# Optimization experiments

Measured on AMD Instinct MI355X. Metric: run time of the kernel, lower is better.

Reference implementation:

```python
import jax, jax.numpy as jnp
import numpy as np

B, S, E, H = 2, 2048, 1024, 16
HD = E // H


def setup_inputs() -> dict:
    key = jax.random.key(0)
    ks = jax.random.split(key, 9)
    s = 1.0 / np.sqrt(E)
    return {
        "x": jax.random.normal(ks[0], (B, S, E), dtype=jnp.float32),
        "wq": jax.random.uniform(ks[1], (E, E), jnp.float32, -s, s),
        "bq": jax.random.uniform(ks[2], (E,), jnp.float32, -s, s),
        "wk": jax.random.uniform(ks[3], (E, E), jnp.float32, -s, s),
        "bk": jax.random.uniform(ks[4], (E,), jnp.float32, -s, s),
        "wv": jax.random.uniform(ks[5], (E, E), jnp.float32, -s, s),
        "bv": jax.random.uniform(ks[6], (E,), jnp.float32, -s, s),
        "wo": jax.random.uniform(ks[7], (E, E), jnp.float32, -s, s),
        "bo": jax.random.uniform(ks[8], (E,), jnp.float32, -s, s),
    }


def reference(x, wq, bq, wk, bk, wv, bv, wo, bo):
    b, s, e = x.shape
    # QKV projections, reshape to [b, h, s, hd]
    def proj(w, bias):
        y = jnp.einsum('bse,ef->bsf', x, w.T) + bias
        return y.reshape(b, s, H, HD).transpose(0, 2, 1, 3)
    q = proj(wq, bq)
    k = proj(wk, bk)
    v = proj(wv, bv)
    score = jnp.einsum('bhqd,bhkd->bhqk', q, k) / jnp.sqrt(jnp.float32(HD))
    # original: exp(x)/sum(exp(x)) + 1e-8  == softmax(x) + 1e-8
    attn = jax.nn.softmax(score, axis=-1) + 1e-8
    out = jnp.einsum('bhqk,bhkd->bhqd', attn, v)
    out = out.transpose(0, 2, 1, 3).reshape(b, s, e)
    return jnp.einsum('bse,ef->bsf', out, wo.T) + bo
```

## Files before the change

### kernel.cpp

```cpp
#include <hip/hip_runtime.h>
#include <hip/hip_bf16.h>
#include <cstdint>

#define SS 2048
#define EE 1024
#define HH 16
#define HDD 64

typedef __attribute__((ext_vector_type(8))) __bf16 bf16x8;
typedef __attribute__((ext_vector_type(4))) float f32x4;

#define MFMA16(a, b, c) __builtin_amdgcn_mfma_f32_16x16x32_bf16((a), (b), (c), 0, 0, 0)

__device__ __forceinline__ unsigned short f2bf(float f) {
    unsigned int u = __builtin_bit_cast(unsigned int, f);
    u += 0x7FFFu + ((u >> 16) & 1u);
    return (unsigned short)(u >> 16);
}

__device__ __forceinline__ void gll16(const unsigned short* g, unsigned short* l) {
    __builtin_amdgcn_global_load_lds(
        (__attribute__((address_space(1))) unsigned int*)g,
        (__attribute__((address_space(3))) unsigned int*)l, 16, 0, 0);
}

__global__ __launch_bounds__(256) void cvt_all(
    const float* __restrict__ x, const float* __restrict__ wq, const float* __restrict__ wk,
    const float* __restrict__ wv, const float* __restrict__ wo,
    unsigned short* __restrict__ xb, unsigned short* __restrict__ wqb, unsigned short* __restrict__ wkb,
    unsigned short* __restrict__ wvb, unsigned short* __restrict__ wob) {
    int idx = blockIdx.x * 256 + threadIdx.x;
    int i4 = idx << 2;
    const float* src;
    unsigned short* dst;
    int off;
    if (i4 < 4194304) { src = x; dst = xb; off = i4; }
    else {
        int w = (i4 - 4194304) >> 20;
        off = (i4 - 4194304) & 1048575;
        if (w == 0) { src = wq; dst = wqb; }
        else if (w == 1) { src = wk; dst = wkb; }
        else if (w == 2) { src = wv; dst = wvb; }
        else { src = wo; dst = wob; }
    }
    float4 v = *(const float4*)&src[off];
    unsigned int p0 = (unsigned int)f2bf(v.x) | ((unsigned int)f2bf(v.y) << 16);
    unsigned int p1 = (unsigned int)f2bf(v.z) | ((unsigned int)f2bf(v.w) << 16);
    uint2 u; u.x = p0; u.y = p1;
    *(uint2*)&dst[off] = u;
}

template <int MODE>
__device__ __forceinline__ void gemm_core(
    const unsigned short* __restrict__ A, const unsigned short* __restrict__ W,
    const float* __restrict__ bias, void* __restrict__ out) {
    __shared__ unsigned short lsA[128 * 32];
    __shared__ unsigned short lsB[128 * 32];
    const int t = threadIdx.x;
    const int lane = t & 63, l15 = lane & 15, quad = lane >> 4;
    const int wave = t >> 6;
    const int wm = (wave >> 1) * 64, wn = (wave & 1) * 64;
    const int bm = blockIdx.y * 128, bn = blockIdx.x * 128;

    const int cg = ((t & 3) ^ ((t >> 3) & 3)) * 8;
    const unsigned short* ga = A + (size_t)(bm + (t >> 2)) * 1024 + cg;
    const unsigned short* gb = W + (size_t)(bn + (t >> 2)) * 1024 + cg;

    f32x4 acc[4][4];
    for (int i = 0; i < 4; i++)
        for (int j = 0; j < 4; j++) acc[i][j] = (f32x4){0.f, 0.f, 0.f, 0.f};

    const int swz = (l15 >> 1) & 3;

    for (int k0 = 0; k0 < 1024; k0 += 32) {
        gll16(ga + k0, &lsA[t * 8]);
        gll16(ga + k0 + 64 * 1024, &lsA[2048 + t * 8]);
        gll16(gb + k0, &lsB[t * 8]);
        gll16(gb + k0 + 64 * 1024, &lsB[2048 + t * 8]);
        __syncthreads();
        bf16x8 af[4], bfr[4];
        for (int i = 0; i < 4; i++)
            af[i] = *(const bf16x8*)&lsA[(wm + i * 16 + l15) * 32 + ((quad ^ swz) * 8)];
        for (int j = 0; j < 4; j++)
            bfr[j] = *(const bf16x8*)&lsB[(wn + j * 16 + l15) * 32 + ((quad ^ swz) * 8)];
        for (int i = 0; i < 4; i++)
            for (int j = 0; j < 4; j++) acc[i][j] = MFMA16(af[i], bfr[j], acc[i][j]);
        __syncthreads();
    }

    for (int j = 0; j < 4; j++) {
        int n = bn + wn + j * 16 + l15;
        float bj = bias[n];
        for (int i = 0; i < 4; i++) {
            int mbase = bm + wm + i * 16 + quad * 4;
            for (int rg = 0; rg < 4; rg++) {
                float val = acc[i][j][rg] + bj;
                int m = mbase + rg;
                if (MODE == 0) {
                    ((unsigned short*)out)[(((size_t)(m >> 11) * HH + (n >> 6)) * SS + (m & 2047)) * HDD + (n & 63)] = f2bf(val);
                } else {
                    ((float*)out)[(size_t)m * 1024 + n] = val;
                }
            }
        }
    }
}

__global__ __launch_bounds__(256) void gemm_qkv(
    const unsigned short* __restrict__ xb,
    const unsigned short* __restrict__ wqb, const unsigned short* __restrict__ wkb,
    const unsigned short* __restrict__ wvb,
    const float* __restrict__ bq, const float* __restrict__ bk, const float* __restrict__ bv,
    unsigned short* qb, unsigned short* kb, unsigned short* vb) {
    const unsigned short* W;
    const float* bias;
    unsigned short* out;
    if (blockIdx.z == 0) { W = wqb; bias = bq; out = qb; }
    else if (blockIdx.z == 1) { W = wkb; bias = bk; out = kb; }
    else { W = wvb; bias = bv; out = vb; }
    gemm_core<0>(xb, W, bias, out);
}

__global__ __launch_bounds__(256) void gemm_out(
    const unsigned short* __restrict__ ob, const unsigned short* __restrict__ wob,
    const float* __restrict__ bo, float* __restrict__ out) {
    gemm_core<1>(ob, wob, bo, out);
}

__global__ __launch_bounds__(256) void transpose_v(
    const unsigned short* __restrict__ vb, unsigned short* __restrict__ vtb) {
    __shared__ unsigned short tile[64 * 66];
    const int t = threadIdx.x;
    const int bh = blockIdx.y, st = blockIdx.x;
    const size_t base = (size_t)bh * (SS * HDD);
    const int c = (t & 7) * 8, r0 = t >> 3;
    for (int it = 0; it < 2; it++) {
        int r = r0 + it * 32;
        uint4 d = *(const uint4*)&vb[base + (size_t)(st * 64 + r) * HDD + c];
        unsigned int* dst = (unsigned int*)&tile[r * 66 + c];
        dst[0] = d.x; dst[1] = d.y; dst[2] = d.z; dst[3] = d.w;
    }
    __syncthreads();
    for (int it = 0; it < 2; it++) {
        int hd = r0 + it * 32;
        unsigned short v0[8];
        for (int k = 0; k < 8; k++) v0[k] = tile[(c + k) * 66 + hd];
        uint4 o;
        o.x = (unsigned int)v0[0] | ((unsigned int)v0[1] << 16);
        o.y = (unsigned int)v0[2] | ((unsigned int)v0[3] << 16);
        o.z = (unsigned int)v0[4] | ((unsigned int)v0[5] << 16);
        o.w = (unsigned int)v0[6] | ((unsigned int)v0[7] << 16);
        *(uint4*)&vtb[base + (size_t)hd * SS + st * 64 + c] = o;
    }
}

#define PSTR 72

__global__ __launch_bounds__(256) void attn_fwd(
    const unsigned short* __restrict__ qb, const unsigned short* __restrict__ kb,
    const unsigned short* __restrict__ vtb, unsigned short* __restrict__ ob) {
    __shared__ unsigned short lsK[64 * 64];
    __shared__ unsigned short lsV[64 * 64];
    __shared__ unsigned short lsP[4 * 32 * PSTR];
    const int t = threadIdx.x, lane = t & 63, l15 = lane & 15, quad = lane >> 4, wave = t >> 6;
    const int bh = blockIdx.y, qt = blockIdx.x;
    const size_t hoff = (size_t)bh * (SS * HDD);
    const float C = 0.125f * 1.44269504088896f;

    bf16x8 qf[2][2];
    const int qrow = qt * 128 + wave * 32;
    for (int i = 0; i < 2; i++)
        for (int ks = 0; ks < 2; ks++) {
            bf16x8 raw = *(const bf16x8*)&qb[hoff + (size_t)(qrow + i * 16 + l15) * HDD + ks * 32 + quad * 8];
            unsigned short tmp[8];
            *(bf16x8*)tmp = raw;
            for (int j = 0; j < 8; j++) {
                float f = __builtin_bit_cast(float, (unsigned int)tmp[j] << 16);
                tmp[j] = f2bf(f * C);
            }
            qf[i][ks] = *(const bf16x8*)tmp;
        }

    unsigned short onesbuf[8];
    for (int j = 0; j < 8; j++) onesbuf[j] = 0x3F80;
    const bf16x8 onesf = *(const bf16x8*)onesbuf;

    f32x4 lacc[2];
    f32x4 o[2][4];
    for (int i = 0; i < 2; i++) {
        lacc[i] = (f32x4){0.f, 0.f, 0.f, 0.f};
        for (int jh = 0; jh < 4; jh++) o[i][jh] = (f32x4){0.f, 0.f, 0.f, 0.f};
    }

    const int cg = (((t & 7) ^ ((t >> 3) & 7))) * 8;
    const unsigned short* gk = kb + hoff + (size_t)(t >> 3) * HDD + cg;
    const unsigned short* gv = vtb + hoff + (size_t)(t >> 3) * SS + cg;
    const int pbase = wave * 32 * PSTR;
    const int sw = l15 & 7;

    for (int kt = 0; kt < 32; kt++) {
        gll16(gk + (size_t)kt * 64 * HDD, &lsK[t * 8]);
        gll16(gk + (size_t)kt * 64 * HDD + 32 * HDD, &lsK[2048 + t * 8]);
        gll16(gv + kt * 64, &lsV[t * 8]);
        gll16(gv + kt * 64 + 32 * SS, &lsV[2048 + t * 8]);
        __syncthreads();

        bf16x8 kfr[4][2];
        for (int j = 0; j < 4; j++)
            for (int ks = 0; ks < 2; ks++)
                kfr[j][ks] = *(const bf16x8*)&lsK[(j * 16 + l15) * 64 + (((ks * 4 + quad) ^ sw) * 8)];

        f32x4 st[4][2];
        for (int j = 0; j < 4; j++)
            for (int i = 0; i < 2; i++) {
                f32x4 z = (f32x4){0.f, 0.f, 0.f, 0.f};
                z = MFMA16(kfr[j][0], qf[i][0], z);
                z = MFMA16(kfr[j][1], qf[i][1], z);
                st[j][i] = z;
            }

        for (int j = 0; j < 4; j++)
            for (int i = 0; i < 2; i++) {
                float e0 = __builtin_amdgcn_exp2f(st[j][i][0]);
                float e1 = __builtin_amdgcn_exp2f(st[j][i][1]);
                float e2 = __builtin_amdgcn_exp2f(st[j][i][2]);
                float e3 = __builtin_amdgcn_exp2f(st[j][i][3]);
                uint2 w;
                w.x = (__builtin_bit_cast(unsigned int, e0) >> 16) |
                      (__builtin_bit_cast(unsigned int, e1) & 0xFFFF0000u);
                w.y = (__builtin_bit_cast(unsigned int, e2) >> 16) |
                      (__builtin_bit_cast(unsigned int, e3) & 0xFFFF0000u);
                *(uint2*)&lsP[pbase + (i * 16 + l15) * PSTR + j * 16 + quad * 4] = w;
            }

        bf16x8 pf[2][2], vf[4][2];
        for (int i = 0; i < 2; i++)
            for (int ks = 0; ks < 2; ks++)
                pf[i][ks] = *(const bf16x8*)&lsP[pbase + (i * 16 + l15) * PSTR + ks * 32 + quad * 8];
        for (int jh = 0; jh < 4; jh++)
            for (int ks = 0; ks < 2; ks++)
                vf[jh][ks] = *(const bf16x8*)&lsV[(jh * 16 + l15) * 64 + (((ks * 4 + quad) ^ sw) * 8)];
        for (int i = 0; i < 2; i++) {
            for (int jh = 0; jh < 4; jh++) {
                o[i][jh] = MFMA16(pf[i][0], vf[jh][0], o[i][jh]);
                o[i][jh] = MFMA16(pf[i][1], vf[jh][1], o[i][jh]);
            }
            lacc[i] = MFMA16(pf[i][0], onesf, lacc[i]);
            lacc[i] = MFMA16(pf[i][1], onesf, lacc[i]);
        }
        __syncthreads();
    }

    const int b = bh >> 4, h = bh & 15;
    for (int i = 0; i < 2; i++)
        for (int rg = 0; rg < 4; rg++) {
            float inv = 1.f / lacc[i][rg];
            int srow = qt * 128 + wave * 32 + i * 16 + quad * 4 + rg;
            size_t rowoff = ((size_t)b * SS + srow) * EE + h * 64;
            for (int jh = 0; jh < 4; jh++)
                ob[rowoff + jh * 16 + l15] = f2bf(o[i][jh][rg] * inv);
        }
}

extern "C" void kernel_launch(void* const* d_in, const int* in_sizes, int n_in,
                              void* d_out, int out_size, void* d_ws, size_t ws_size,
                              hipStream_t stream) {
    const float* x  = (const float*)d_in[0];
    const float* wq = (const float*)d_in[1];
    const float* bq = (const float*)d_in[2];
    const float* wk = (const float*)d_in[3];
    const float* bk = (const float*)d_in[4];
    const float* wv = (const float*)d_in[5];
    const float* bv = (const float*)d_in[6];
    const float* wo = (const float*)d_in[7];
    const float* bo = (const float*)d_in[8];

    char* ws = (char*)d_ws;
    unsigned short* xb  = (unsigned short*)(ws + 0);
    unsigned short* wqb = (unsigned short*)(ws + 8388608);
    unsigned short* wkb = (unsigned short*)(ws + 10485760);
    unsigned short* wvb = (unsigned short*)(ws + 12582912);
    unsigned short* wob = (unsigned short*)(ws + 14680064);
    unsigned short* qb  = (unsigned short*)(ws + 16777216);
    unsigned short* kb  = (unsigned short*)(ws + 25165824);
    unsigned short* vb  = (unsigned short*)(ws + 33554432);
    unsigned short* vtb = (unsigned short*)(ws + 41943040);
    unsigned short* ob  = xb;

    cvt_all<<<8192, 256, 0, stream>>>(x, wq, wk, wv, wo, xb, wqb, wkb, wvb, wob);
    gemm_qkv<<<dim3(8, 32, 3), 256, 0, stream>>>(xb, wqb, wkb, wvb, bq, bk, bv, qb, kb, vb);
    transpose_v<<<dim3(32, 32), 256, 0, stream>>>(vb, vtb);
    attn_fwd<<<dim3(16, 32), 256, 0, stream>>>(qb, kb, vtb, ob);
    gemm_out<<<dim3(8, 32), 256, 0, stream>>>(ob, wob, bo, (float*)d_out);
}
```

Before: 222.8 us.

## Fuse V transpose into QKV GEMM epilogue, remap blocks, narrow output GEMM tiles

The QKV GEMM now writes V directly in transposed [b,h,hd,s] layout using packed 4-element stores, which removes the separate transpose_v kernel and its round trip through global memory. All three main kernels switch to 1D grids with a block-index remapping that spreads consecutive blocks across 8 groups, likely to balance work across XCDs and L2 caches. The output GEMM uses 128x64 tiles, giving 512 blocks instead of 256 for better CU occupancy. The cost is uncoalesced strided stores in the V epilogue and smaller per-block reuse in the output GEMM.

```diff
diff --git a/kernel.cpp b/kernel.cpp
--- a/kernel.cpp
+++ b/kernel.cpp
@@ -50,25 +50,25 @@
     *(uint2*)&dst[off] = u;
 }
 
-template <int MODE>
+template <int MODE, int BNT>
 __device__ __forceinline__ void gemm_core(
     const unsigned short* __restrict__ A, const unsigned short* __restrict__ W,
-    const float* __restrict__ bias, void* __restrict__ out) {
+    const float* __restrict__ bias, void* __restrict__ out, int bm, int bn) {
+    constexpr int JT = BNT / 32;
     __shared__ unsigned short lsA[128 * 32];
-    __shared__ unsigned short lsB[128 * 32];
+    __shared__ unsigned short lsB[BNT * 32];
     const int t = threadIdx.x;
     const int lane = t & 63, l15 = lane & 15, quad = lane >> 4;
     const int wave = t >> 6;
-    const int wm = (wave >> 1) * 64, wn = (wave & 1) * 64;
-    const int bm = blockIdx.y * 128, bn = blockIdx.x * 128;
+    const int wm = (wave >> 1) * 64, wn = (wave & 1) * (BNT / 2);
 
     const int cg = ((t & 3) ^ ((t >> 3) & 3)) * 8;
     const unsigned short* ga = A + (size_t)(bm + (t >> 2)) * 1024 + cg;
     const unsigned short* gb = W + (size_t)(bn + (t >> 2)) * 1024 + cg;
 
-    f32x4 acc[4][4];
+    f32x4 acc[4][JT];
     for (int i = 0; i < 4; i++)
-        for (int j = 0; j < 4; j++) acc[i][j] = (f32x4){0.f, 0.f, 0.f, 0.f};
+        for (int j = 0; j < JT; j++) acc[i][j] = (f32x4){0.f, 0.f, 0.f, 0.f};
 
     const int swz = (l15 >> 1) & 3;
 
@@ -76,30 +76,40 @@
         gll16(ga + k0, &lsA[t * 8]);
         gll16(ga + k0 + 64 * 1024, &lsA[2048 + t * 8]);
         gll16(gb + k0, &lsB[t * 8]);
-        gll16(gb + k0 + 64 * 1024, &lsB[2048 + t * 8]);
-        __syncthreads();
-        bf16x8 af[4], bfr[4];
+        if (BNT == 128) gll16(gb + k0 + 64 * 1024, &lsB[2048 + t * 8]);
+        __syncthreads();
+        bf16x8 af[4], bfr[JT];
         for (int i = 0; i < 4; i++)
             af[i] = *(const bf16x8*)&lsA[(wm + i * 16 + l15) * 32 + ((quad ^ swz) * 8)];
-        for (int j = 0; j < 4; j++)
+        for (int j = 0; j < JT; j++)
             bfr[j] = *(const bf16x8*)&lsB[(wn + j * 16 + l15) * 32 + ((quad ^ swz) * 8)];
         for (int i = 0; i < 4; i++)
-            for (int j = 0; j < 4; j++) acc[i][j] = MFMA16(af[i], bfr[j], acc[i][j]);
-        __syncthreads();
-    }
-
-    for (int j = 0; j < 4; j++) {
+            for (int j = 0; j < JT; j++) acc[i][j] = MFMA16(af[i], bfr[j], acc[i][j]);
+        __syncthreads();
+    }
+
+    for (int j = 0; j < JT; j++) {
         int n = bn + wn + j * 16 + l15;
         float bj = bias[n];
         for (int i = 0; i < 4; i++) {
-            int mbase = bm + wm + i * 16 + quad * 4;
-            for (int rg = 0; rg < 4; rg++) {
-                float val = acc[i][j][rg] + bj;
-                int m = mbase + rg;
-                if (MODE == 0) {
-                    ((unsigned short*)out)[(((size_t)(m >> 11) * HH + (n >> 6)) * SS + (m & 2047)) * HDD + (n & 63)] = f2bf(val);
-                } else {
-                    ((float*)out)[(size_t)m * 1024 + n] = val;
+            int m0 = bm + wm + i * 16 + quad * 4;
+            if (MODE == 2) {
+                float v0 = acc[i][j][0] + bj, v1 = acc[i][j][1] + bj;
+                float v2 = acc[i][j][2] + bj, v3 = acc[i][j][3] + bj;
+                uint2 w;
+                w.x = (unsigned int)f2bf(v0) | ((unsigned int)f2bf(v1) << 16);
+                w.y = (unsigned int)f2bf(v2) | ((unsigned int)f2bf(v3) << 16);
+                size_t addr = (((size_t)(m0 >> 11) * HH + (n >> 6)) * HDD + (n & 63)) * SS + (m0 & 2047);
+                *(uint2*)&((unsigned short*)out)[addr] = w;
+            } else {
+                for (int rg = 0; rg < 4; rg++) {
+                    float val = acc[i][j][rg] + bj;
+                    int m = m0 + rg;
+                    if (MODE == 0) {
+                        ((unsigned short*)out)[(((size_t)(m >> 11) * HH + (n >> 6)) * SS + (m & 2047)) * HDD + (n & 63)] = f2bf(val);
+                    } else {
+                        ((float*)out)[(size_t)m * 1024 + n] = val;
+                    }
                 }
             }
         }
@@ -111,47 +121,25 @@
     const unsigned short* __restrict__ wqb, const unsigned short* __restrict__ wkb,
     const unsigned short* __restrict__ wvb,
     const float* __restrict__ bq, const float* __restrict__ bk, const float* __restrict__ bv,
-    unsigned short* qb, unsigned short* kb, unsigned short* vb) {
-    const unsigned short* W;
-    const float* bias;
-    unsigned short* out;
-    if (blockIdx.z == 0) { W = wqb; bias = bq; out = qb; }
-    else if (blockIdx.z == 1) { W = wkb; bias = bk; out = kb; }
-    else { W = wvb; bias = bv; out = vb; }
-    gemm_core<0>(xb, W, bias, out);
+    unsigned short* qb, unsigned short* kb, unsigned short* vtb) {
+    const int blk = blockIdx.x;
+    const int u = blk & 7, r = blk >> 3;
+    const int by = u + 8 * (r & 3);
+    const int rest = r >> 2;
+    const int bx = rest & 7, z = rest >> 3;
+    if (z == 0)      gemm_core<0, 128>(xb, wqb, bq, qb,  by * 128, bx * 128);
+    else if (z == 1) gemm_core<0, 128>(xb, wkb, bk, kb,  by * 128, bx * 128);
+    else             gemm_core<2, 128>(xb, wvb, bv, vtb, by * 128, bx * 128);
 }
 
 __global__ __launch_bounds__(256) void gemm_out(
     const unsigned short* __restrict__ ob, const unsigned short* __restrict__ wob,
     const float* __restrict__ bo, float* __restrict__ out) {
-    gemm_core<1>(ob, wob, bo, out);
-}
-
-__global__ __launch_bounds__(256) void transpose_v(
-    const unsigned short* __restrict__ vb, unsigned short* __restrict__ vtb) {
-    __shared__ unsigned short tile[64 * 66];
-    const int t = threadIdx.x;
-    const int bh = blockIdx.y, st = blockIdx.x;
-    const size_t base = (size_t)bh * (SS * HDD);
-    const int c = (t & 7) * 8, r0 = t >> 3;
-    for (int it = 0; it < 2; it++) {
-        int r = r0 + it * 32;
-        uint4 d = *(const uint4*)&vb[base + (size_t)(st * 64 + r) * HDD + c];
-        unsigned int* dst = (unsigned int*)&tile[r * 66 + c];
-        dst[0] = d.x; dst[1] = d.y; dst[2] = d.z; dst[3] = d.w;
-    }
-    __syncthreads();
-    for (int it = 0; it < 2; it++) {
-        int hd = r0 + it * 32;
-        unsigned short v0[8];
-        for (int k = 0; k < 8; k++) v0[k] = tile[(c + k) * 66 + hd];
-        uint4 o;
-        o.x = (unsigned int)v0[0] | ((unsigned int)v0[1] << 16);
-        o.y = (unsigned int)v0[2] | ((unsigned int)v0[3] << 16);
-        o.z = (unsigned int)v0[4] | ((unsigned int)v0[5] << 16);
-        o.w = (unsigned int)v0[6] | ((unsigned int)v0[7] << 16);
-        *(uint4*)&vtb[base + (size_t)hd * SS + st * 64 + c] = o;
-    }
+    const int blk = blockIdx.x;
+    const int u = blk & 7, r = blk >> 3;
+    const int by = u + 8 * (r & 3);
+    const int bx = r >> 2;
+    gemm_core<1, 64>(ob, wob, bo, out, by * 128, bx * 64);
 }
 
 #define PSTR 72
@@ -163,7 +151,10 @@
     __shared__ unsigned short lsV[64 * 64];
     __shared__ unsigned short lsP[4 * 32 * PSTR];
     const int t = threadIdx.x, lane = t & 63, l15 = lane & 15, quad = lane >> 4, wave = t >> 6;
-    const int bh = blockIdx.y, qt = blockIdx.x;
+    const int blk = blockIdx.x;
+    const int u = blk & 7, r = blk >> 3;
+    const int bh = u + 8 * (r & 3);
+    const int qt = r >> 2;
     const size_t hoff = (size_t)bh * (SS * HDD);
     const float C = 0.125f * 1.44269504088896f;
 
@@ -283,13 +274,11 @@
     unsigned short* wob = (unsigned short*)(ws + 14680064);
     unsigned short* qb  = (unsigned short*)(ws + 16777216);
     unsigned short* kb  = (unsigned short*)(ws + 25165824);
-    unsigned short* vb  = (unsigned short*)(ws + 33554432);
-    unsigned short* vtb = (unsigned short*)(ws + 41943040);
+    unsigned short* vtb = (unsigned short*)(ws + 33554432);
     unsigned short* ob  = xb;
 
     cvt_all<<<8192, 256, 0, stream>>>(x, wq, wk, wv, wo, xb, wqb, wkb, wvb, wob);
-    gemm_qkv<<<dim3(8, 32, 3), 256, 0, stream>>>(xb, wqb, wkb, wvb, bq, bk, bv, qb, kb, vb);
-    transpose_v<<<dim3(32, 32), 256, 0, stream>>>(vb, vtb);
-    attn_fwd<<<dim3(16, 32), 256, 0, stream>>>(qb, kb, vtb, ob);
-    gemm_out<<<dim3(8, 32), 256, 0, stream>>>(ob, wob, bo, (float*)d_out);
-}
+    gemm_qkv<<<768, 256, 0, stream>>>(xb, wqb, wkb, wvb, bq, bk, bv, qb, kb, vtb);
+    attn_fwd<<<512, 256, 0, stream>>>(qb, kb, vtb, ob);
+    gemm_out<<<512, 256, 0, stream>>>(ob, wob, bo, (float*)d_out);
+}
```

Result: faster. 204.9 us (-8.0%).
